# Performance work log

Hardware: AMD Instinct MI355X
Metric: run time of the kernel (lower is better)

The kernel has to match this reference:

```python
import jax, jax.numpy as jnp
import numpy as np

# ---- module constants (from init_kwargs) ----
GRID = np.array([160, 160, 160], dtype=np.int32)
CENTER = np.array([0.0, 0.0, 0.0], dtype=np.float32)
SIZE = np.array([200.0, 200.0, 200.0], dtype=np.float32)
KERNEL_WIDTH = 3.0
N_SAMPLES = 128   # line-integral samples per LOR (ray-driven TOR approximation)
N_LORS = 50000

_CORNERS = [(dx, dy, dz) for dx in (0, 1) for dy in (0, 1) for dz in (0, 1)]


def _sample_line(lors, grid, center, size, n_samples, dtype):
    """lors: [N,6] (p1 xyz, p2 xyz). Returns base voxel idx i0 [N,S,3],
    trilinear fracs w [N,S,3], per-sample step length [N]."""
    p1, p2 = lors[:, 0:3], lors[:, 3:6]
    t = (jnp.arange(n_samples, dtype=dtype) + 0.5) / n_samples          # [S]
    pos = p1[:, None, :] + t[None, :, None] * (p2 - p1)[:, None, :]     # [N,S,3]
    step = jnp.linalg.norm(p2 - p1, axis=-1) / n_samples                # [N]
    gridf = grid.astype(np.float32)
    vsize = size / gridf
    origin = center - 0.5 * size
    f = (pos - origin) / vsize - 0.5        # continuous voxel-center coords
    f = jnp.clip(f, 0.0, gridf - 1.0)
    i0 = jnp.clip(jnp.floor(f).astype(jnp.int32), 0, grid - 2)          # [N,S,3]
    w = f - i0.astype(dtype)                                            # [N,S,3]
    return i0, w, step


def _corner_weight(w, c):
    dx, dy, dz = c
    wx = w[..., 0] if dx else 1.0 - w[..., 0]
    wy = w[..., 1] if dy else 1.0 - w[..., 1]
    wz = w[..., 2] if dz else 1.0 - w[..., 2]
    return wx * wy * wz


def projection(lors, image, grid, center, size, kernel_width):
    """Ray-driven line integrals through image. lors [N,6] -> [N]."""
    i0, w, step = _sample_line(lors, grid, center, size, N_SAMPLES, image.dtype)
    val = jnp.zeros(i0.shape[:2], image.dtype)   # [N,S]
    for c in _CORNERS:
        dx, dy, dz = c
        val = val + _corner_weight(w, c) * image[i0[..., 0] + dx,
                                                 i0[..., 1] + dy,
                                                 i0[..., 2] + dz]
    return kernel_width * step * val.sum(axis=1)  # [N]


def backprojection(image, grid, lors, center, size, line_integral, kernel_width):
    """Scatter line_integral back along the same rays -> volume like image."""
    i0, w, step = _sample_line(lors, grid, center, size, N_SAMPLES, image.dtype)
    contrib = (kernel_width * line_integral * step)[:, None]  # [N,1] -> bcast [N,S]
    bp = jnp.zeros(image.shape, image.dtype)
    for c in _CORNERS:
        dx, dy, dz = c
        bp = bp.at[i0[..., 0] + dx, i0[..., 1] + dy, i0[..., 2] + dz].add(
            _corner_weight(w, c) * contrib)
    return bp


def _tor_step(image, efficiency_map, xlors, ylors, zlors):
    imgz = image
    imgx = jnp.transpose(imgz, (2, 0, 1))
    imgy = jnp.transpose(imgz, (1, 0, 2))
    xl = jnp.transpose(xlors)  # [N,6]
    yl = jnp.transpose(ylors)
    zl = jnp.transpose(zlors)

    # z-direction (native axis order)
    pz = projection(zl, imgz, GRID, CENTER, SIZE, KERNEL_WIDTH)
    bpz = backprojection(imgz, GRID, zl, CENTER, SIZE, pz, KERNEL_WIDTH)

    # x-direction: permuted frame (y, z, x)
    gx = GRID[[1, 2, 0]]; cx = CENTER[[1, 2, 0]]; sx = SIZE[[1, 2, 0]]
    px = projection(xl, imgx, gx, cx, sx, KERNEL_WIDTH)
    bpx = backprojection(imgx, gx, xl, cx, sx, px, KERNEL_WIDTH)
    bpxt = jnp.transpose(bpx, (1, 2, 0))

    # y-direction: permuted frame (x, z, y)
    gy = GRID[[0, 2, 1]]; cy = CENTER[[0, 2, 1]]; sy = SIZE[[0, 2, 1]]
    py = projection(yl, imgy, gy, cy, sy, KERNEL_WIDTH)
    bpy = backprojection(imgy, gy, yl, cy, sy, py, KERNEL_WIDTH)
    bpyt = jnp.transpose(bpy, (1, 0, 2))

    return imgz * efficiency_map * (bpxt + bpyt + bpz)


def setup_inputs() -> dict:
    key = jax.random.key(0)
    k_img, k_eff, kx, ky, kz = jax.random.split(key, 5)
    image = jax.random.uniform(k_img, tuple(GRID), dtype=jnp.float32)
    effmap = jax.random.uniform(k_eff, tuple(GRID), dtype=jnp.float32)
    lo = jnp.asarray(np.concatenate([CENTER - 0.5 * SIZE] * 2), jnp.float32)   # [6]
    span = jnp.asarray(np.concatenate([SIZE] * 2), jnp.float32)                # [6]
    def mk(k):
        u = jax.random.uniform(k, (6, N_LORS), dtype=jnp.float32)
        return u * span[:, None] + lo[:, None]
    return {"image": image, "efficiency_map": effmap,
            "xlors": mk(kx), "ylors": mk(ky), "zlors": mk(kz)}


def reference(image, efficiency_map, xlors, ylors, zlors):
    return _tor_step(image, efficiency_map, xlors, ylors, zlors)
```

## Files before the change

### kernel.cpp

```cpp
#include <hip/hip_runtime.h>

#define NL 50000
#define NS 128
#define G 160
#define GSQ (160*160)
#define GCUBE (160*160*160)
#define NRB 196
#define NBINS (G*2)
#define ENT_CAP 11500000

struct RayParam { float4 a, b; };

__device__ __forceinline__ void lds_add(float* p, float v) {
    atomicAdd(p, v);
}

__device__ __forceinline__ float frcp(float x) {
#if __has_builtin(__builtin_amdgcn_rcpf)
    return __builtin_amdgcn_rcpf(x);
#else
    return 1.0f / x;
#endif
}

__device__ __forceinline__ void coordf(float pos, int& i, float& w) {
    float f = (pos + 100.0f) * 0.8f - 0.5f;
    f = fminf(fmaxf(f, 0.0f), 159.0f);
    int ii = (int)f; ii = ii > 158 ? 158 : ii;
    i = ii; w = f - (float)ii;
}

__device__ __forceinline__ int cnt_for(float A, float B, float rB, int p, int& slo_out) {
    const float glo = (p <= 1)   ? -1.0f  : (float)(p - 1);
    const float ghi = (p >= 158) ? 160.0f : (float)(p + 1);
    int slo, shi;
    if (B == 0.0f) {
        if (A < glo || A > ghi) { slo_out = 0; return 0; }
        slo = 0; shi = NS - 1;
    } else {
        const float t1 = (glo - A) * rB, t2 = (ghi - A) * rB;
        const float tlo = fminf(t1, t2), thi = fmaxf(t1, t2);
        float slof = ceilf (tlo * (float)NS - 0.75f);
        float shif = floorf(thi * (float)NS - 0.25f);
        slof = fminf(fmaxf(slof,  0.0f), 127.0f);
        shif = fminf(fmaxf(shif, -1.0f), 127.0f);
        slo = (int)slof; shi = (int)shif;
    }
    slo_out = slo;
    return shi - slo + 1;
}

__device__ __forceinline__ void halves_for(
    float A, float B, float rB, int p, float AR, float BR,
    int& lo0, int& n0, int& lo1, int& n1)
{
    lo0 = lo1 = 0; n0 = n1 = 0;
    int slo; const int c = cnt_for(A, B, rB, p, slo);
    if (c <= 0) return;
    const int shi = slo + c - 1;
    if (BR == 0.0f) {
        if (AR < 80.0f) { lo0 = slo; n0 = c; } else { lo1 = slo; n1 = c; }
        return;
    }
    float sstar = ((80.0f - AR) * frcp(BR)) * (float)NS - 0.5f;
    sstar = fminf(fmaxf(sstar, -300.0f), 300.0f);
    float lo0f, hi0f, lo1f, hi1f;
    if (BR > 0.0f) {
        lo0f = (float)slo;  hi0f = fminf((float)shi, floorf(sstar) + 1.0f);
        lo1f = fmaxf((float)slo, ceilf(sstar) - 1.0f);  hi1f = (float)shi;
    } else {
        lo1f = (float)slo;  hi1f = fminf((float)shi, floorf(sstar) + 1.0f);
        lo0f = fmaxf((float)slo, ceilf(sstar) - 1.0f);  hi0f = (float)shi;
    }
    lo0 = (int)lo0f; n0 = (int)hi0f - lo0 + 1; if (n0 < 0) n0 = 0;
    lo1 = (int)lo1f; n1 = (int)hi1f - lo1 + 1; if (n1 < 0) n1 = 0;
}

__device__ __forceinline__ void plane_range(float A, float B, int& plo, int& phi) {
    const float f0 = A + B * (0.5f / NS);
    const float f1 = A + B * (((float)NS - 0.5f) / NS);
    const float fmn = fminf(f0, f1), fmx = fmaxf(f0, f1);
    plo = (int)fmaxf(ceilf (fmn - 1.01f), 0.0f);
    phi = (int)fminf(floorf(fmx + 1.01f), 159.0f);
}

template<int PA, int PB, int PC, int QS, int QR, int QC>
__device__ __forceinline__ void proj_body(
    const float* __restrict__ img,
    const float* __restrict__ lors,
    float* __restrict__ contrib,
    RayParam* __restrict__ params,
    int sa, int sb, int bx)
{
    const int wave = threadIdx.x >> 6;
    const int lane = threadIdx.x & 63;
    const int lor  = bx * 4 + wave;

    const float p1x = lors[0*NL + lor];
    const float p1y = lors[1*NL + lor];
    const float p1z = lors[2*NL + lor];
    const float dxv = lors[3*NL + lor] - p1x;
    const float dyv = lors[4*NL + lor] - p1y;
    const float dzv = lors[5*NL + lor] - p1z;
    const float len  = sqrtf(dxv*dxv + dyv*dyv + dzv*dzv);
    const float step = len * (1.0f/NS);

    float2 P00[2], P01[2], P10[2], P11[2];
    float waq[2], wbq[2], wcq[2];

    #pragma unroll
    for (int q = 0; q < 2; ++q) {
        const int s = lane + q*64;
        const float t = ((float)s + 0.5f) * (1.0f/NS);
        const float pos[3] = { p1x + t*dxv, p1y + t*dyv, p1z + t*dzv };
        int ia, ib, ic; float wa, wb, wc;
        coordf(pos[PA], ia, wa);
        coordf(pos[PB], ib, wb);
        coordf(pos[PC], ic, wc);
        const float* g = img + ia*sa + ib*sb + ic;
        __builtin_memcpy(&P00[q], g,            8);
        __builtin_memcpy(&P01[q], g + sb,       8);
        __builtin_memcpy(&P10[q], g + sa,       8);
        __builtin_memcpy(&P11[q], g + sa + sb,  8);
        waq[q] = wa; wbq[q] = wb; wcq[q] = wc;
    }

    float sum = 0.0f;
    #pragma unroll
    for (int q = 0; q < 2; ++q) {
        const float wa = waq[q], wb = wbq[q], wc = wcq[q];
        const float c00 = P00[q].x + wc*(P00[q].y - P00[q].x);
        const float c01 = P01[q].x + wc*(P01[q].y - P01[q].x);
        const float c10 = P10[q].x + wc*(P10[q].y - P10[q].x);
        const float c11 = P11[q].x + wc*(P11[q].y - P11[q].x);
        const float c0  = c00 + wb*(c01 - c00);
        const float c1  = c10 + wb*(c11 - c10);
        sum += c0 + wa*(c1 - c0);
    }

    #pragma unroll
    for (int off = 32; off > 0; off >>= 1)
        sum += __shfl_xor(sum, off, 64);

    if (lane == 0) {
        const float cb = 9.0f * step * step * sum;
        contrib[lor] = cb;
        if (params) {
            const float P1v[3] = { p1x, p1y, p1z };
            const float DVv[3] = { dxv, dyv, dzv };
            float4 a, b;
            a.x = (P1v[QS] + 100.0f)*0.8f - 0.5f;  a.y = DVv[QS]*0.8f;
            a.z = (P1v[QR] + 100.0f)*0.8f - 0.5f;  a.w = DVv[QR]*0.8f;
            b.x = (P1v[QC] + 100.0f)*0.8f - 0.5f;  b.y = DVv[QC]*0.8f;
            b.z = cb;                               b.w = 0.0f;
            params[lor].a = a;
            params[lor].b = b;
        }
    }
}

__global__ __launch_bounds__(256) void proj_all(
    const float* __restrict__ img,
    const float* __restrict__ xl, const float* __restrict__ yl,
    const float* __restrict__ zl,
    float* __restrict__ cz, float* __restrict__ cx, float* __restrict__ cy,
    RayParam* __restrict__ params)
{
    const int bx = blockIdx.x;
    if (blockIdx.y == 0)
        proj_body<0,1,2, 0,1,2>(img, zl, cz, params ? params        : nullptr, GSQ, G, bx);
    else if (blockIdx.y == 1)
        proj_body<1,2,0, 1,2,0>(img, xl, cx, params ? params +   NL : nullptr, GSQ, G, bx);
    else
        proj_body<0,1,2, 1,0,2>(img, yl, cy, params ? params + 2*NL : nullptr, G, GSQ, bx);
}

__global__ __launch_bounds__(256) void bin_count(
    const RayParam* __restrict__ params, int* __restrict__ totals)
{
    const int rb = blockIdx.x, pass = blockIdx.y;
    __shared__ int cnt[NBINS];
    for (int i = threadIdx.x; i < NBINS; i += 256) cnt[i] = 0;
    __syncthreads();

    const int r = rb*256 + threadIdx.x;
    if (r < NL) {
        const float4 a = params[pass*NL + r].a;
        const float A = a.x, B = a.y, AR = a.z, BR = a.w;
        int plo, phi; plane_range(A, B, plo, phi);
        const float rB = frcp(B);
        for (int p = plo; p <= phi; ++p) {
            int lo0, n0, lo1, n1;
            halves_for(A, B, rB, p, AR, BR, lo0, n0, lo1, n1);
            if (n0 > 0) atomicAdd(&cnt[p*2    ], (n0 + 7) >> 3);
            if (n1 > 0) atomicAdd(&cnt[p*2 + 1], (n1 + 7) >> 3);
        }
    }
    __syncthreads();
    for (int i = threadIdx.x; i < NBINS; i += 256)
        if (cnt[i]) atomicAdd(&totals[i], cnt[i]);
}

__global__ __launch_bounds__(512) void scan320(
    const int* __restrict__ totals, int* __restrict__ offsets,
    int* __restrict__ cur)
{
    __shared__ int v[NBINS];
    const int tid = threadIdx.x;
    int mine = 0;
    if (tid < NBINS) { mine = totals[tid]; v[tid] = mine; }
    __syncthreads();
    for (int off = 1; off < NBINS; off <<= 1) {
        int x = 0;
        if (tid < NBINS && tid >= off) x = v[tid - off];
        __syncthreads();
        if (tid < NBINS) v[tid] += x;
        __syncthreads();
    }
    if (tid < NBINS) {
        const int excl = v[tid] - mine;
        offsets[tid] = excl;
        cur[tid]     = excl;
    }
    if (tid == 0) offsets[NBINS] = v[NBINS-1];
}

__global__ __launch_bounds__(256) void bin_write(
    const RayParam* __restrict__ params, int* __restrict__ cur,
    unsigned* __restrict__ entries)
{
    const int rb = blockIdx.x, pass = blockIdx.y;
    __shared__ int cnt[NBINS];
    __shared__ int base[NBINS];
    for (int i = threadIdx.x; i < NBINS; i += 256) cnt[i] = 0;
    __syncthreads();

    const int r = rb*256 + threadIdx.x;
    float A = 0, B = 0, AR = 0, BR = 0, rB = 0;
    int plo = 0, phi = -1;
    if (r < NL) {
        const float4 a = params[pass*NL + r].a;
        A = a.x; B = a.y; AR = a.z; BR = a.w;
        plane_range(A, B, plo, phi);
        rB = frcp(B);
        for (int p = plo; p <= phi; ++p) {
            int lo0, n0, lo1, n1;
            halves_for(A, B, rB, p, AR, BR, lo0, n0, lo1, n1);
            if (n0 > 0) atomicAdd(&cnt[p*2    ], (n0 + 7) >> 3);
            if (n1 > 0) atomicAdd(&cnt[p*2 + 1], (n1 + 7) >> 3);
        }
    }
    __syncthreads();
    for (int i = threadIdx.x; i < NBINS; i += 256) {
        const int c = cnt[i];
        base[i] = c ? atomicAdd(&cur[i], c) : 0;
    }
    __syncthreads();
    for (int i = threadIdx.x; i < NBINS; i += 256) cnt[i] = 0;
    __syncthreads();

    if (r < NL) {
        for (int p = plo; p <= phi; ++p) {
            int lo0, n0, lo1, n1;
            halves_for(A, B, rB, p, AR, BR, lo0, n0, lo1, n1);
            #pragma unroll
            for (int h = 0; h < 2; ++h) {
                const int lo = h ? lo1 : lo0;
                const int n  = h ? n1  : n0;
                if (n > 0) {
                    const int bin = p*2 + h;
                    const int ke = (n + 7) >> 3;
                    const int gb = base[bin] + atomicAdd(&cnt[bin], ke);
                    for (int e = 0; e < ke; ++e) {
                        const int s0 = lo + e*8;
                        const int nn = (n - e*8) < 8 ? (n - e*8) : 8;
                        const unsigned enc = (unsigned)r | ((unsigned)s0 << 17)
                                           | ((unsigned)(nn-1) << 24)
                                           | ((unsigned)pass << 27);
                        if (gb + e < ENT_CAP) entries[gb + e] = enc;
                    }
                }
            }
        }
    }
}

__global__ __launch_bounds__(512) void bp_half(
    const RayParam* __restrict__ params, const int* __restrict__ offsets,
    const unsigned* __restrict__ entries,
    float* __restrict__ out)
{
    __shared__ float tile[81*G];
    const int b   = blockIdx.x;
    const int c   = blockIdx.y;
    const int p   = b >> 1;
    const int h   = b & 1;
    const int tid = threadIdx.x;
    const int rowbase = 80 * h;

    for (int j = tid; j < 81*G; j += 512) tile[j] = 0.0f;
    __syncthreads();

    int s0 = offsets[b];
    int e0 = offsets[b+1];
    if (e0 > ENT_CAP) e0 = ENT_CAP;
    if (s0 > e0) s0 = e0;
    const int n  = e0 - s0;
    const int cs = s0 + (n *  c     ) / 2;
    const int ce = s0 + (n * (c + 1)) / 2;

    int e = cs + tid;
    unsigned enc = 0; RayParam rp;
    if (e < ce) {
        enc = entries[e];
        rp  = params[(enc >> 27)*NL + (enc & 0x1FFFF)];
    }

    int   pk  = -1;
    float a00 = 0.0f, a01 = 0.0f, a10 = 0.0f, a11 = 0.0f;

    while (e < ce) {
        const int en = e + 512;
        unsigned encN = 0;
        if (en < ce) encN = entries[en];

        const int ss = (enc >> 17) & 0x7F;
        const int nn = ((enc >> 24) & 0x7) + 1;
        const float A = rp.a.x, B = rp.a.y, AR = rp.a.z, BR = rp.a.w;
        const float AC = rp.b.x, BC = rp.b.y, cb = rp.b.z;

        for (int i = 0; i < nn; ++i) {
            const float t = ((float)(ss + i) + 0.5f) * (1.0f/NS);
            float fA = A + B*t;
            fA = fminf(fmaxf(fA, 0.0f), 159.0f);
            int ia = (int)fA; ia = ia > 158 ? 158 : ia;
            const float wa = fA - (float)ia;
            float fa;
            if (ia == p)          fa = 1.0f - wa;
            else if (ia == p - 1) fa = wa;
            else                  fa = -1.0f;

            float fR = AR + BR*t;
            fR = fminf(fmaxf(fR, 0.0f), 159.0f);
            int ib = (int)fR; ib = ib > 158 ? 158 : ib;
            const int rl = ib - rowbase;

            if (fa >= 0.0f && rl >= 0 && rl <= 79) {
                float fC = AC + BC*t;
                fC = fminf(fmaxf(fC, 0.0f), 159.0f);
                int ic = (int)fC; ic = ic > 158 ? 158 : ic;
                const float wb = fR - (float)ib;
                const float wc = fC - (float)ic;
                const float v  = fa * cb;
                const float v0 = v * (1.0f - wb), v1 = v * wb;
                const int key = rl*G + ic;
                if (key != pk) {
                    if (pk >= 0) {
                        float* q = tile + pk;
                        const int d = key - pk;
                        if (d == 1) {
                            lds_add(q,     a00);
                            lds_add(q + G, a10);
                            a00 = a01; a10 = a11; a01 = 0.0f; a11 = 0.0f;
                        } else if (d == -1) {
                            lds_add(q + 1,     a01);
                            lds_add(q + G + 1, a11);
                            a01 = a00; a11 = a10; a00 = 0.0f; a10 = 0.0f;
                        } else if (d == G) {
                            lds_add(q,     a00);
                            lds_add(q + 1, a01);
                            a00 = a10; a01 = a11; a10 = 0.0f; a11 = 0.0f;
                        } else if (d == -G) {
                            lds_add(q + G,     a10);
                            lds_add(q + G + 1, a11);
                            a10 = a00; a11 = a01; a00 = 0.0f; a01 = 0.0f;
                        } else {
                            lds_add(q,         a00);
                            lds_add(q + 1,     a01);
                            lds_add(q + G,     a10);
                            lds_add(q + G + 1, a11);
                            a00 = 0.0f; a01 = 0.0f; a10 = 0.0f; a11 = 0.0f;
                        }
                    }
                    pk = key;
                }
                a00 += v0 * (1.0f - wc);
                a01 += v0 * wc;
                a10 += v1 * (1.0f - wc);
                a11 += v1 * wc;
            }
        }

        if (en < ce)
            rp = params[(encN >> 27)*NL + (encN & 0x1FFFF)];
        enc = encN; e = en;
    }

    if (pk >= 0) {
        float* q = tile + pk;
        lds_add(q,         a00);
        lds_add(q + 1,     a01);
        lds_add(q + G,     a10);
        lds_add(q + G + 1, a11);
    }
    __syncthreads();

    const int nrows = h ? 80 : 81;
    float* dst = out + (size_t)p * GSQ + (size_t)rowbase * G;
    for (int j = tid; j < nrows*G; j += 512) {
#if __has_builtin(__builtin_amdgcn_global_atomic_fadd_f32)
        unsafeAtomicAdd(&dst[j], tile[j]);
#else
        atomicAdd(&dst[j], tile[j]);
#endif
    }
}

__global__ __launch_bounds__(256) void finalize_mul(
    const float4* __restrict__ img, const float4* __restrict__ eff,
    float4* __restrict__ out)
{
    const int i = blockIdx.x * 256 + threadIdx.x;
    const float4 a = img[i];
    const float4 e = eff[i];
    float4 o = out[i];
    o.x *= a.x * e.x;
    o.y *= a.y * e.y;
    o.z *= a.z * e.z;
    o.w *= a.w * e.w;
    out[i] = o;
}

template<int PS, int PR, int PC2>
__device__ __forceinline__ void slab_accum(
    float* __restrict__ plane,
    const float* __restrict__ lors,
    const float* __restrict__ contrib,
    int p, int wave, int lane, int nwaves)
{
    for (int base = wave*64; base < NL; base += nwaves*64) {
        const int r = base + lane;
        float A = 0.f, B = 0.f, AR = 0.f, BR = 0.f, AC = 0.f, BC = 0.f, cb = 0.f;
        int slo = 0, cnt = 0;
        if (r < NL) {
            const float q0 = lors[0*NL + r], q1 = lors[1*NL + r], q2 = lors[2*NL + r];
            const float d0 = lors[3*NL + r] - q0;
            const float d1 = lors[4*NL + r] - q1;
            const float d2 = lors[5*NL + r] - q2;
            const float P1[3] = { q0, q1, q2 };
            const float DV[3] = { d0, d1, d2 };
            A  = (P1[PS]  + 100.0f)*0.8f - 0.5f;  B  = DV[PS]*0.8f;
            AR = (P1[PR]  + 100.0f)*0.8f - 0.5f;  BR = DV[PR]*0.8f;
            AC = (P1[PC2] + 100.0f)*0.8f - 0.5f;  BC = DV[PC2]*0.8f;
            cb = contrib[r];
            const float rB = frcp(B);
            cnt = cnt_for(A, B, rB, p, slo);
            if (cnt < 0) cnt = 0;
        }

        int pref = cnt;
        #pragma unroll
        for (int off = 1; off < 64; off <<= 1) {
            const int nsh = __shfl_up(pref, off, 64);
            if (lane >= off) pref += nsh;
        }
        const int total = __shfl(pref, 63, 64);
        const int start = pref - cnt;

        for (int k0 = 0; k0 < total; k0 += 64) {
            const int k  = k0 + lane;
            const int kc = k < total ? k : total - 1;

            int j = 0;
            #pragma unroll
            for (int stp = 32; stp >= 1; stp >>= 1) {
                const int cand = j + stp;
                const int sc = __shfl(start, cand, 64);
                if (cand < 64 && sc <= kc) j = cand;
            }

            const int   sj  = __shfl(slo,   j, 64);
            const int   stj = __shfl(start, j, 64);
            const float Aj  = __shfl(A,  j, 64);
            const float Bj  = __shfl(B,  j, 64);
            const float ARj = __shfl(AR, j, 64);
            const float BRj = __shfl(BR, j, 64);
            const float ACj = __shfl(AC, j, 64);
            const float BCj = __shfl(BC, j, 64);
            const float cbj = __shfl(cb, j, 64);

            const int s = sj + (kc - stj);
            const float t = ((float)s + 0.5f) * (1.0f/NS);
            float fA = Aj + Bj * t;
            fA = fminf(fmaxf(fA, 0.0f), 159.0f);
            int ia = (int)fA; ia = ia > 158 ? 158 : ia;
            const float wa = fA - (float)ia;
            float fa;
            if (ia == p)          fa = 1.0f - wa;
            else if (ia == p - 1) fa = wa;
            else                  fa = -1.0f;

            float fR = ARj + BRj * t;
            float fC = ACj + BCj * t;
            fR = fminf(fmaxf(fR, 0.0f), 159.0f);
            fC = fminf(fmaxf(fC, 0.0f), 159.0f);
            int ib = (int)fR; ib = ib > 158 ? 158 : ib;
            int ic = (int)fC; ic = ic > 158 ? 158 : ic;
            const float wb = fR - (float)ib;
            const float wc = fC - (float)ic;

            if (k < total && fa >= 0.0f) {
                const float v  = fa * cbj;
                const float v0 = v * (1.0f - wb), v1 = v * wb;
                float* q = plane + ib*G + ic;
                lds_add(q,         v0 * (1.0f - wc));
                lds_add(q + 1,     v0 * wc);
                lds_add(q + G,     v1 * (1.0f - wc));
                lds_add(q + G + 1, v1 * wc);
            }
        }
    }
}

__global__ __launch_bounds__(1024) void bp_fused(
    const float* __restrict__ img, const float* __restrict__ eff,
    const float* __restrict__ zl, const float* __restrict__ xl,
    const float* __restrict__ yl,
    const float* __restrict__ cz, const float* __restrict__ cx,
    const float* __restrict__ cy,
    float* __restrict__ out)
{
    __shared__ float plane[GSQ];
    const int p    = blockIdx.x;
    const int tid  = threadIdx.x;
    const int wave = tid >> 6;
    const int lane = tid & 63;

    for (int j = tid; j < GSQ; j += 1024) plane[j] = 0.0f;
    __syncthreads();

    slab_accum<0,1,2>(plane, zl, cz, p, wave, lane, 16);
    slab_accum<1,2,0>(plane, xl, cx, p, wave, lane, 16);
    slab_accum<1,0,2>(plane, yl, cy, p, wave, lane, 16);

    __syncthreads();

    const int pbase = p * GSQ;
    for (int j = tid; j < GSQ; j += 1024) {
        const int idx = pbase + j;
        out[idx] = plane[j] * img[idx] * eff[idx];
    }
}

extern "C" void kernel_launch(void* const* d_in, const int* in_sizes, int n_in,
                              void* d_out, int out_size, void* d_ws, size_t ws_size,
                              hipStream_t stream) {
    const float* img = (const float*)d_in[0];
    const float* eff = (const float*)d_in[1];
    const float* xl  = (const float*)d_in[2];
    const float* yl  = (const float*)d_in[3];
    const float* zl  = (const float*)d_in[4];
    float* out = (float*)d_out;

    const size_t CONTRIB_B = (size_t)3*NL*sizeof(float);
    const size_t PARAMS_B  = (size_t)3*NL*sizeof(RayParam);
    const size_t TOT_B     = (size_t)NBINS*sizeof(int);
    const size_t OFFS_B    = (size_t)(NBINS+1)*sizeof(int);
    const size_t CUR_B     = (size_t)NBINS*sizeof(int);
    const size_t ENT_B     = (size_t)ENT_CAP*sizeof(unsigned);

    char* w = (char*)d_ws;
    float*    cz      = (float*)w;
    float*    cx      = cz + NL;
    float*    cy      = cx + NL;
    RayParam* params  = (RayParam*)(w + CONTRIB_B);
    int*      totals  = (int*)(w + CONTRIB_B + PARAMS_B);
    int*      offsets = (int*)(w + CONTRIB_B + PARAMS_B + TOT_B);
    int*      cur     = (int*)(w + CONTRIB_B + PARAMS_B + TOT_B + OFFS_B);
    unsigned* entries = (unsigned*)(w + CONTRIB_B + PARAMS_B + TOT_B + OFFS_B + CUR_B);

    const bool binned =
        ws_size >= CONTRIB_B + PARAMS_B + TOT_B + OFFS_B + CUR_B + ENT_B;

    proj_all<<<dim3(NL/4, 3), dim3(256), 0, stream>>>(
        img, xl, yl, zl, cz, cx, cy, binned ? params : nullptr);

    if (binned) {
        hipMemsetAsync(out, 0, (size_t)GCUBE * sizeof(float), stream);
        hipMemsetAsync(totals, 0, TOT_B, stream);
        bin_count<<<dim3(NRB, 3), dim3(256), 0, stream>>>(params, totals);
        scan320  <<<dim3(1),      dim3(512), 0, stream>>>(totals, offsets, cur);
        bin_write<<<dim3(NRB, 3), dim3(256), 0, stream>>>(params, cur, entries);
        bp_half  <<<dim3(NBINS,2),dim3(512), 0, stream>>>(params, offsets, entries, out);
        finalize_mul<<<dim3(GCUBE/4/256), dim3(256), 0, stream>>>(
            (const float4*)img, (const float4*)eff, (float4*)out);
    } else {
        bp_fused<<<dim3(G), dim3(1024), 0, stream>>>(
            img, eff, zl, xl, yl, cz, cx, cy, out);
    }
}
```

Measured before the change: 1.139 ms.

## Fuse bin counting into projection kernel and split backprojection bins three ways

Bin counting moves out of its own kernel and into the projection kernel. Each wave now computes its ray's plane range and spreads the per-plane bin counts across its lanes into shared memory, then flushes them to global totals. This removes a kernel launch and the re-read of the ray parameters. Separately, each backprojection bin's entry list is split across three blocks instead of two for more parallelism, at the cost of more global atomic traffic into the output volume.

```diff
diff --git a/kernel.cpp b/kernel.cpp
--- a/kernel.cpp
+++ b/kernel.cpp
@@ -90,6 +90,7 @@
     const float* __restrict__ lors,
     float* __restrict__ contrib,
     RayParam* __restrict__ params,
+    int* __restrict__ cnt,
     int sa, int sb, int bx)
 {
     const int wave = threadIdx.x >> 6;
@@ -142,19 +143,35 @@
     for (int off = 32; off > 0; off >>= 1)
         sum += __shfl_xor(sum, off, 64);
 
+    const float P1v[3] = { p1x, p1y, p1z };
+    const float DVv[3] = { dxv, dyv, dzv };
+    const float A  = (P1v[QS] + 100.0f)*0.8f - 0.5f;
+    const float B  = DVv[QS]*0.8f;
+    const float AR = (P1v[QR] + 100.0f)*0.8f - 0.5f;
+    const float BR = DVv[QR]*0.8f;
+    const float AC = (P1v[QC] + 100.0f)*0.8f - 0.5f;
+    const float BC = DVv[QC]*0.8f;
+
     if (lane == 0) {
         const float cb = 9.0f * step * step * sum;
         contrib[lor] = cb;
         if (params) {
-            const float P1v[3] = { p1x, p1y, p1z };
-            const float DVv[3] = { dxv, dyv, dzv };
             float4 a, b;
-            a.x = (P1v[QS] + 100.0f)*0.8f - 0.5f;  a.y = DVv[QS]*0.8f;
-            a.z = (P1v[QR] + 100.0f)*0.8f - 0.5f;  a.w = DVv[QR]*0.8f;
-            b.x = (P1v[QC] + 100.0f)*0.8f - 0.5f;  b.y = DVv[QC]*0.8f;
-            b.z = cb;                               b.w = 0.0f;
+            a.x = A;  a.y = B;  a.z = AR; a.w = BR;
+            b.x = AC; b.y = BC; b.z = cb; b.w = 0.0f;
             params[lor].a = a;
             params[lor].b = b;
+        }
+    }
+
+    if (cnt) {
+        int plo, phi; plane_range(A, B, plo, phi);
+        const float rB = frcp(B);
+        for (int p = plo + lane; p <= phi; p += 64) {
+            int lo0, n0, lo1, n1;
+            halves_for(A, B, rB, p, AR, BR, lo0, n0, lo1, n1);
+            if (n0 > 0) atomicAdd(&cnt[p*2    ], (n0 + 7) >> 3);
+            if (n1 > 0) atomicAdd(&cnt[p*2 + 1], (n1 + 7) >> 3);
         }
     }
 }
@@ -164,41 +181,29 @@
     const float* __restrict__ xl, const float* __restrict__ yl,
     const float* __restrict__ zl,
     float* __restrict__ cz, float* __restrict__ cx, float* __restrict__ cy,
-    RayParam* __restrict__ params)
-{
+    RayParam* __restrict__ params, int* __restrict__ totals)
+{
+    __shared__ int cnt[NBINS];
+    const bool counting = (params != nullptr);
+    if (counting) {
+        for (int i = threadIdx.x; i < NBINS; i += 256) cnt[i] = 0;
+        __syncthreads();
+    }
+    int* cp = counting ? cnt : nullptr;
+
     const int bx = blockIdx.x;
     if (blockIdx.y == 0)
-        proj_body<0,1,2, 0,1,2>(img, zl, cz, params ? params        : nullptr, GSQ, G, bx);
+        proj_body<0,1,2, 0,1,2>(img, zl, cz, params ? params        : nullptr, cp, GSQ, G, bx);
     else if (blockIdx.y == 1)
-        proj_body<1,2,0, 1,2,0>(img, xl, cx, params ? params +   NL : nullptr, GSQ, G, bx);
+        proj_body<1,2,0, 1,2,0>(img, xl, cx, params ? params +   NL : nullptr, cp, GSQ, G, bx);
     else
-        proj_body<0,1,2, 1,0,2>(img, yl, cy, params ? params + 2*NL : nullptr, G, GSQ, bx);
-}
-
-__global__ __launch_bounds__(256) void bin_count(
-    const RayParam* __restrict__ params, int* __restrict__ totals)
-{
-    const int rb = blockIdx.x, pass = blockIdx.y;
-    __shared__ int cnt[NBINS];
-    for (int i = threadIdx.x; i < NBINS; i += 256) cnt[i] = 0;
-    __syncthreads();
-
-    const int r = rb*256 + threadIdx.x;
-    if (r < NL) {
-        const float4 a = params[pass*NL + r].a;
-        const float A = a.x, B = a.y, AR = a.z, BR = a.w;
-        int plo, phi; plane_range(A, B, plo, phi);
-        const float rB = frcp(B);
-        for (int p = plo; p <= phi; ++p) {
-            int lo0, n0, lo1, n1;
-            halves_for(A, B, rB, p, AR, BR, lo0, n0, lo1, n1);
-            if (n0 > 0) atomicAdd(&cnt[p*2    ], (n0 + 7) >> 3);
-            if (n1 > 0) atomicAdd(&cnt[p*2 + 1], (n1 + 7) >> 3);
-        }
-    }
-    __syncthreads();
-    for (int i = threadIdx.x; i < NBINS; i += 256)
-        if (cnt[i]) atomicAdd(&totals[i], cnt[i]);
+        proj_body<0,1,2, 1,0,2>(img, yl, cy, params ? params + 2*NL : nullptr, cp, G, GSQ, bx);
+
+    if (counting) {
+        __syncthreads();
+        for (int i = threadIdx.x; i < NBINS; i += 256)
+            if (cnt[i]) atomicAdd(&totals[i], cnt[i]);
+    }
 }
 
 __global__ __launch_bounds__(512) void scan320(
@@ -306,8 +311,8 @@
     if (e0 > ENT_CAP) e0 = ENT_CAP;
     if (s0 > e0) s0 = e0;
     const int n  = e0 - s0;
-    const int cs = s0 + (n *  c     ) / 2;
-    const int ce = s0 + (n * (c + 1)) / 2;
+    const int cs = s0 + (int)(((long long)n *  c     ) / 3);
+    const int ce = s0 + (int)(((long long)n * (c + 1)) / 3);
 
     int e = cs + tid;
     unsigned enc = 0; RayParam rp;
@@ -582,16 +587,19 @@
     const bool binned =
         ws_size >= CONTRIB_B + PARAMS_B + TOT_B + OFFS_B + CUR_B + ENT_B;
 
+    if (binned) {
+        hipMemsetAsync(totals, 0, TOT_B, stream);
+        hipMemsetAsync(out, 0, (size_t)GCUBE * sizeof(float), stream);
+    }
+
     proj_all<<<dim3(NL/4, 3), dim3(256), 0, stream>>>(
-        img, xl, yl, zl, cz, cx, cy, binned ? params : nullptr);
+        img, xl, yl, zl, cz, cx, cy, binned ? params : nullptr,
+        binned ? totals : nullptr);
 
     if (binned) {
-        hipMemsetAsync(out, 0, (size_t)GCUBE * sizeof(float), stream);
-        hipMemsetAsync(totals, 0, TOT_B, stream);
-        bin_count<<<dim3(NRB, 3), dim3(256), 0, stream>>>(params, totals);
         scan320  <<<dim3(1),      dim3(512), 0, stream>>>(totals, offsets, cur);
         bin_write<<<dim3(NRB, 3), dim3(256), 0, stream>>>(params, cur, entries);
-        bp_half  <<<dim3(NBINS,2),dim3(512), 0, stream>>>(params, offsets, entries, out);
+        bp_half  <<<dim3(NBINS,3),dim3(512), 0, stream>>>(params, offsets, entries, out);
         finalize_mul<<<dim3(GCUBE/4/256), dim3(256), 0, stream>>>(
             (const float4*)img, (const float4*)eff, (float4*)out);
     } else {
```

Measured after the change: 1.549 ms. 36.0% more time.
